# Optimization experiments

Hardware: AMD Instinct MI355X
Metric: run time of the kernel (lower is better)

Reference implementation:

```python
import jax, jax.numpy as jnp
import numpy as np
from jax import lax

B, N, C = 8, 2000, 81
MAX_INST = 100
MIN_CONF = 0.7
NMS_THR = 0.3
WINDOW = jnp.array([0.0, 0.0, 1.0, 1.0], jnp.float32)  # y1, x1, y2, x2
BBOX_STD = jnp.array([0.1, 0.1, 0.2, 0.2], jnp.float32)


def setup_inputs() -> dict:
    key = jax.random.key(0)
    k1, k2, k3 = jax.random.split(key, 3)
    # build valid boxes: sample coordinate pairs and sort so y1<=y2, x1<=x2
    yx = jax.random.uniform(k1, (B, N, 2, 2), dtype=jnp.float32)
    mins, maxs = yx.min(axis=2), yx.max(axis=2)
    rois = jnp.stack([mins[..., 0], mins[..., 1], maxs[..., 0], maxs[..., 1]], axis=-1)
    probs = jax.random.uniform(k2, (B, N, C), dtype=jnp.float32)
    deltas = jax.random.normal(k3, (B, N, C, 4), dtype=jnp.float32) * 0.5
    return {"rois": rois, "probs": probs, "deltas": deltas}


def _apply_box_deltas(boxes, deltas):
    # boxes: [N,4] (y1,x1,y2,x2); deltas: [N,4] (dy,dx,log_dh,log_dw)
    h = boxes[:, 2] - boxes[:, 0]
    w = boxes[:, 3] - boxes[:, 1]
    cy = boxes[:, 0] + 0.5 * h + deltas[:, 0] * h
    cx = boxes[:, 1] + 0.5 * w + deltas[:, 1] * w
    h = h * jnp.exp(deltas[:, 2])
    w = w * jnp.exp(deltas[:, 3])
    return jnp.stack([cy - 0.5 * h, cx - 0.5 * w, cy + 0.5 * h, cx + 0.5 * w], axis=1)


def _clip_boxes(boxes, window):
    wy1, wx1, wy2, wx2 = window
    y1 = jnp.clip(boxes[:, 0], wy1, wy2)
    x1 = jnp.clip(boxes[:, 1], wx1, wx2)
    y2 = jnp.clip(boxes[:, 2], wy1, wy2)
    x2 = jnp.clip(boxes[:, 3], wx1, wx2)
    return jnp.stack([y1, x1, y2, x2], axis=1)


def _pairwise_iou(boxes):
    # boxes: [N,4] -> [N,N]
    y1, x1, y2, x2 = boxes[:, 0], boxes[:, 1], boxes[:, 2], boxes[:, 3]
    area = (y2 - y1) * (x2 - x1)
    iy1 = jnp.maximum(y1[:, None], y1[None, :])
    ix1 = jnp.maximum(x1[:, None], x1[None, :])
    iy2 = jnp.minimum(y2[:, None], y2[None, :])
    ix2 = jnp.minimum(x2[:, None], x2[None, :])
    inter = jnp.maximum(iy2 - iy1, 0.0) * jnp.maximum(ix2 - ix1, 0.0)
    union = area[:, None] + area[None, :] - inter
    return inter / jnp.maximum(union, 1e-12)


def _refine_one(rois, probs, deltas):
    # rois [N,4], probs [N,C], deltas [N,C,4]
    class_ids = jnp.argmax(probs, axis=1)                      # [N]
    rng = jnp.arange(N)
    class_scores = probs[rng, class_ids]                       # [N]
    deltas_specific = deltas[rng, class_ids]                   # [N,4]
    refined = _apply_box_deltas(rois, deltas_specific * BBOX_STD)
    refined = _clip_boxes(refined, WINDOW)

    valid = (class_ids > 0) & (class_scores >= MIN_CONF)

    # sort by score descending (invalid entries pushed to the end)
    order = jnp.argsort(-jnp.where(valid, class_scores, -jnp.inf))
    boxes_s = refined[order]
    scores_s = class_scores[order]
    cls_s = class_ids[order]
    valid_s = valid[order]

    # per-class greedy NMS: suppress only within the same class
    iou = _pairwise_iou(boxes_s)                               # [N,N]
    suppress_mat = (iou > NMS_THR) & (cls_s[:, None] == cls_s[None, :])
    lower = jnp.arange(N)

    def body(i, keep):
        sup = suppress_mat[i] & keep[i] & (lower > i)
        return keep & ~sup

    keep = lax.fori_loop(0, N, body, valid_s)

    # per-class cap at MAX_INST (mirrors max_output_size in tf NMS)
    onehot = jax.nn.one_hot(cls_s, C, dtype=jnp.int32) * keep.astype(jnp.int32)[:, None]
    rank = jnp.cumsum(onehot, axis=0)[lower, cls_s]            # inclusive per-class rank
    keep = keep & (rank <= MAX_INST)

    # global top-k by score among kept, zero-padded
    final_scores = jnp.where(keep, scores_s, -jnp.inf)
    _, top_idx = lax.top_k(final_scores, MAX_INST)
    valid_top = keep[top_idx]
    box_out = jnp.where(valid_top[:, None], boxes_s[top_idx], 0.0)
    cls_out = jnp.where(valid_top, cls_s[top_idx].astype(jnp.float32), 0.0)
    sc_out = jnp.where(valid_top, scores_s[top_idx], 0.0)
    return jnp.concatenate([box_out, cls_out[:, None], sc_out[:, None]], axis=1)  # [MAX_INST,6]


def reference(rois, probs, deltas):
    return jax.vmap(_refine_one)(rois, probs, deltas)  # [B, MAX_INST, 6]
```

## Files before the change

### kernel.cpp

```cpp
#include <hip/hip_runtime.h>
#include <math.h>

#define BB 8
#define NN 2000
#define CC 81
#define NCLS 80
#define MAXI 100
#define MCLS 128
#define WCAP 128
#define KCAP 2048

static constexpr float kMinConf = 0.7f;
static constexpr float kNmsThr  = 0.3f;


__device__ __forceinline__ unsigned long long mkey(float s, int i) {
    return ((unsigned long long)__float_as_uint(s) << 32) | (unsigned int)(~(unsigned int)i);
}

__device__ __forceinline__ bool iou_gt_thr(float4 a, float aarea, float4 t) {
    float iy1 = fmaxf(a.x, t.x), ix1 = fmaxf(a.y, t.y);
    float iy2 = fminf(a.z, t.z), ix2 = fminf(a.w, t.w);
    float inter = fmaxf(iy2 - iy1, 0.f) * fmaxf(ix2 - ix1, 0.f);
    float tarea = (t.z - t.x) * (t.w - t.y);
    float uni = fmaxf(aarea + tarea - inter, 1e-12f);
    return inter > kNmsThr * uni;
}

__global__ void kA_refine(const float* __restrict__ rois,
                          const float* __restrict__ probs,
                          const float* __restrict__ deltas,
                          float* __restrict__ boxes,
                          float* __restrict__ sc,
                          int* __restrict__ cls,
                          float* __restrict__ outz) {
    int gtid = blockIdx.x * blockDim.x + threadIdx.x;
    if (gtid < BB * MAXI * 6) outz[gtid] = 0.f;

    int wid = gtid >> 6;
    int l = gtid & 63;

    const float* p = probs + (size_t)wid * CC;
    float v1 = p[l];
    int   i1 = l;
    int   c2 = l + 64;
    float v2 = (c2 < CC) ? p[c2] : -1.0f;
    float bv; int bi;
    if (v2 > v1) { bv = v2; bi = c2; } else { bv = v1; bi = i1; }

    #pragma unroll
    for (int off = 32; off; off >>= 1) {
        float ov = __shfl_xor(bv, off);
        int   oi = __shfl_xor(bi, off);
        if (ov > bv || (ov == bv && oi < bi)) { bv = ov; bi = oi; }
    }

    if (l == 0) {
        const float4 dl = *(const float4*)(deltas + ((size_t)wid * CC + bi) * 4);
        float dy = dl.x * 0.1f, dx = dl.y * 0.1f, dh = dl.z * 0.2f, dw = dl.w * 0.2f;
        const float4 r = *(const float4*)(rois + (size_t)wid * 4);
        float y1 = r.x, x1 = r.y, y2 = r.z, x2 = r.w;
        float h = y2 - y1, w = x2 - x1;
        float cy = y1 + 0.5f * h + dy * h;
        float cx = x1 + 0.5f * w + dx * w;
        float h2 = h * expf(dh);
        float w2 = w * expf(dw);
        float oy1 = fminf(fmaxf(cy - 0.5f * h2, 0.f), 1.f);
        float ox1 = fminf(fmaxf(cx - 0.5f * w2, 0.f), 1.f);
        float oy2 = fminf(fmaxf(cy + 0.5f * h2, 0.f), 1.f);
        float ox2 = fminf(fmaxf(cx + 0.5f * w2, 0.f), 1.f);
        bool valid = (bi > 0) && (bv >= kMinConf);
        float4 bx; bx.x = oy1; bx.y = ox1; bx.z = oy2; bx.w = ox2;
        ((float4*)boxes)[wid] = bx;
        sc[wid] = bv;
        cls[wid] = valid ? bi : 0;
    }
}

__global__ void __launch_bounds__(256) kB_nms(
        const float* __restrict__ boxes,
        const float* __restrict__ sc,
        const int* __restrict__ cls,
        int* __restrict__ kslot,
        unsigned long long* __restrict__ klist) {
    const int p = blockIdx.x;
    const int b = p / NCLS;
    const int cidx = p % NCLS;
    const int c = cidx + 1;
    const int tid = threadIdx.x;
    const int wv = tid >> 6;
    const int l = tid & 63;

    __shared__ unsigned long long wlist[4][WCAP];
    __shared__ int wcnt[4];
    __shared__ unsigned long long mk[MCLS];
    __shared__ float4 mbox[MCLS];

    const int* cl = cls + (size_t)b * NN;
    const float* ssc = sc + (size_t)b * NN;
    const float4* bxs = (const float4*)boxes + (size_t)b * NN;

    {
        int cnt = 0;
        const int base_row = wv * 500;
        for (int ch = 0; ch < 8; ++ch) {
            int idx = ch * 64 + l;
            bool inq = idx < 500;
            int r = base_row + idx;
            int ci = inq ? cl[r] : 0;
            bool pred = (ci == c);
            unsigned long long mask = __ballot(pred);
            if (pred) {
                int pos = cnt + __popcll(mask & ((1ull << l) - 1ull));
                if (pos < WCAP) wlist[wv][pos] = mkey(ssc[r], r);
            }
            cnt += __popcll(mask);
        }
        if (l == 0) wcnt[wv] = (cnt > WCAP) ? WCAP : cnt;
    }
    __syncthreads();

    int b0 = wcnt[0], b1 = wcnt[1], b2 = wcnt[2], b3 = wcnt[3];
    int myofs = (wv > 0 ? b0 : 0) + (wv > 1 ? b1 : 0) + (wv > 2 ? b2 : 0);
    int myn = wcnt[wv];
    int cnt_all = b0 + b1 + b2 + b3;
    if (cnt_all > MCLS) cnt_all = MCLS;
    if (l < myn && myofs + l < MCLS) mk[myofs + l] = wlist[wv][l];
    if (64 + l < myn && myofs + 64 + l < MCLS) mk[myofs + 64 + l] = wlist[wv][64 + l];
    __syncthreads();

    if (wv != 0) return;
    if (cnt_all == 0) {
        if (l == 0) kslot[b * NCLS + cidx] = 0;
        return;
    }
    const int cnt = cnt_all;

    {
        unsigned long long Ka = (l < cnt) ? mk[l] : 0ull;
        unsigned long long Kb = (64 + l < cnt) ? mk[64 + l] : 0ull;
        int ra = 0, rb = 0;
        for (int t = 0; t < cnt; ++t) {
            unsigned long long kt = mk[t];
            ra += (kt > Ka);
            rb += (kt > Kb);
        }
        if (l < cnt) mk[ra] = Ka;
        if (64 + l < cnt) mk[rb] = Kb;
    }

    for (int t = l; t < cnt; t += 64) {
        int i = (int)(~(unsigned int)mk[t]);
        mbox[t] = bxs[i];
    }

    unsigned long long kept0 = 0ull, kept1 = 0ull;
    {
        bool act = (l < cnt);
        float4 a = mbox[act ? l : 0];
        float aarea = (a.z - a.x) * (a.w - a.y);
        unsigned long long colmask = 0ull;
        int tend = min(64, cnt);
        for (int t = 0; t < tend; ++t) {
            float4 tb = mbox[t];
            if (t < l && act && iou_gt_thr(a, aarea, tb)) colmask |= (1ull << t);
        }
        unsigned long long kept = __ballot(act);
        while (true) {
            bool alive = act && ((colmask & kept) == 0ull);
            unsigned long long k2m = __ballot(alive);
            if (k2m == kept) break;
            kept = k2m;
        }
        kept0 = kept;
    }
    if (cnt > 64) {
        int m = 64 + l;
        bool act = (m < cnt);
        float4 a = mbox[act ? m : 0];
        float aarea = (a.z - a.x) * (a.w - a.y);
        bool presup = false;
        for (int t = 0; t < 64; ++t) {
            if ((kept0 >> t) & 1ull) {
                if (act && iou_gt_thr(a, aarea, mbox[t])) presup = true;
            }
        }
        unsigned long long colmask = 0ull;
        for (int t = 64; t < cnt; ++t) {
            float4 tb = mbox[t];
            if ((t - 64) < l && act && iou_gt_thr(a, aarea, tb)) colmask |= (1ull << (t - 64));
        }
        bool pre = act && !presup;
        unsigned long long kept = __ballot(pre);
        while (true) {
            bool alive = pre && ((colmask & kept) == 0ull);
            unsigned long long k2m = __ballot(alive);
            if (k2m == kept) break;
            kept = k2m;
        }
        kept1 = kept;
    }

    int nk0 = __popcll(kept0), nk1 = __popcll(kept1);
    unsigned long long* slot = klist + ((size_t)b * NCLS + cidx) * MCLS;
    if ((kept0 >> l) & 1ull)
        slot[__popcll(kept0 & ((1ull << l) - 1ull))] = mk[l];
    if (cnt > 64 && ((kept1 >> l) & 1ull))
        slot[nk0 + __popcll(kept1 & ((1ull << l) - 1ull))] = mk[64 + l];
    if (l == 0) kslot[b * NCLS + cidx] = nk0 + nk1;
}

__global__ void __launch_bounds__(512) kC_emit(
        const int* __restrict__ kslot,
        const unsigned long long* __restrict__ klist,
        const float* __restrict__ boxes,
        const int* __restrict__ cls,
        float* __restrict__ out) {
    const int b = blockIdx.x;
    const int tid = threadIdx.x;
    const int wv = tid >> 6;
    const int l = tid & 63;

    __shared__ unsigned long long keys[KCAP];
    __shared__ ulonglong2 cand2[256];
    __shared__ int hist[256];
    __shared__ int sbase[NCLS], scount[NCLS];
    __shared__ int Tsh, tbsh, candn;
    unsigned long long* cand = (unsigned long long*)cand2;

    if (tid < 256) hist[tid] = 0;
    if (tid == 0) candn = 0;

    if (wv == 0) {
        const int* ks = kslot + b * NCLS;
        int ns0 = ks[l];
        int ns1 = (l < NCLS - 64) ? ks[64 + l] : 0;
        int incA = ns0, incB = ns1;
        #pragma unroll
        for (int off = 1; off < 64; off <<= 1) {
            int oa = __shfl_up(incA, off);
            int ob = __shfl_up(incB, off);
            if (l >= off) { incA += oa; incB += ob; }
        }
        int total0 = __shfl(incA, 63);
        int T = total0 + __shfl(incB, 63);
        sbase[l] = incA - ns0;
        scount[l] = ns0;
        if (l < NCLS - 64) { sbase[64 + l] = total0 + incB - ns1; scount[64 + l] = ns1; }
        if (l == 0) Tsh = (T > KCAP) ? KCAP : T;
    }
    __syncthreads();
    const int T = Tsh;
    if (T == 0) return;

    const unsigned long long* kbase = klist + (size_t)b * NCLS * MCLS;
    for (int e = tid; e < NCLS * MCLS; e += 512) {
        unsigned long long v = kbase[e];
        int s = e >> 7, j = e & (MCLS - 1);
        if (j < scount[s]) keys[sbase[s] + j] = v;
    }
    __syncthreads();

    for (int t = tid; t < T; t += 512)
        atomicAdd(&hist[(int)((keys[t] >> 47) & 0xFF)], 1);
    __syncthreads();

    if (wv == 0) {
        int cum = 0, tb = 0, done = 0;
        for (int chunk = 3; chunk >= 0 && !done; --chunk) {
            int bkt = chunk * 64 + (63 - l);
            int s = hist[bkt];
            #pragma unroll
            for (int off = 1; off < 64; off <<= 1) {
                int o = __shfl_up(s, off);
                if (l >= off) s += o;
            }
            int chunktot = __shfl(s, 63);
            if (cum + chunktot >= MAXI) {
                unsigned long long m = __ballot(cum + s >= MAXI);
                int lane = __ffsll((long long)m) - 1;
                tb = chunk * 64 + (63 - lane);
                done = 1;
            } else {
                cum += chunktot;
            }
        }
        if (l == 0) tbsh = done ? tb : 0;
    }
    __syncthreads();
    const int tb = tbsh;

    for (int t = tid; t < ((T + 511) & ~511); t += 512) {
        bool pr = (t < T) && ((int)((keys[t] >> 47) & 0xFF) >= tb);
        unsigned long long m = __ballot(pr);
        int nb = __popcll(m);
        int basew = 0;
        if (l == 0 && nb) basew = atomicAdd(&candn, nb);
        basew = __shfl(basew, 0);
        if (pr) {
            int pos = basew + __popcll(m & ((1ull << l) - 1ull));
            if (pos < 512) cand[pos] = keys[t];
        }
    }
    __syncthreads();
    const int nc = candn;
    if (tid == 0 && nc < 512) cand[nc] = 0ull;
    __syncthreads();

    if (nc <= 512) {
        const int np = (nc + 1) >> 1;
        for (int s = tid; s < nc; s += 512) {
            unsigned long long myk = cand[s];
            int r = 0;
            for (int t = 0; t < np; ++t) {
                ulonglong2 kv = cand2[t];
                r += (int)(kv.x > myk);
                r += (int)(kv.y > myk);
            }
            if (r < MAXI) {
                int i = (int)(~(unsigned int)myk);
                float4 bx = ((const float4*)boxes)[(size_t)b * NN + i];
                float* o = out + ((size_t)b * MAXI + r) * 6;
                o[0] = bx.x; o[1] = bx.y; o[2] = bx.z; o[3] = bx.w;
                o[4] = (float)cls[(size_t)b * NN + i];
                o[5] = __uint_as_float((unsigned int)(myk >> 32));
            }
        }
    } else {
        for (int s = tid; s < T; s += 512) {
            unsigned long long myk = keys[s];
            int r = 0;
            for (int t = 0; t < T; ++t) r += (int)(keys[t] > myk);
            if (r < MAXI) {
                int i = (int)(~(unsigned int)myk);
                float4 bx = ((const float4*)boxes)[(size_t)b * NN + i];
                float* o = out + ((size_t)b * MAXI + r) * 6;
                o[0] = bx.x; o[1] = bx.y; o[2] = bx.z; o[3] = bx.w;
                o[4] = (float)cls[(size_t)b * NN + i];
                o[5] = __uint_as_float((unsigned int)(myk >> 32));
            }
        }
    }
}

extern "C" void kernel_launch(void* const* d_in, const int* in_sizes, int n_in,
                              void* d_out, int out_size, void* d_ws, size_t ws_size,
                              hipStream_t stream) {
    const float* rois   = (const float*)d_in[0];
    const float* probs  = (const float*)d_in[1];
    const float* deltas = (const float*)d_in[2];
    float* outp = (float*)d_out;

    char* ws = (char*)d_ws;
    float* boxes = (float*)(ws + 0);
    float* sc    = (float*)(ws + 256000);
    int*   cls   = (int*)  (ws + 320000);
    int*   kslot = (int*)  (ws + 384000);
    unsigned long long* klist = (unsigned long long*)(ws + 386624);

    {
        int blocks = (BB * NN * 64) / 256;
        kA_refine<<<blocks, 256, 0, stream>>>(rois, probs, deltas, boxes, sc, cls, outp);
    }
    {
        kB_nms<<<BB * NCLS, 256, 0, stream>>>(boxes, sc, cls, kslot, klist);
    }
    {
        kC_emit<<<BB, 512, 0, stream>>>(kslot, klist, boxes, cls, outp);
    }
}
```

Baseline: 35.37 us.

## Fuse NMS and emit kernels using release-store flags and spin-waiting emit blocks

Merges the per-class NMS kernel and the per-batch emit kernel into one launch. The emit blocks are appended after the NMS blocks and spin on per-class counters, which are initialised to -1 in the refine kernel and published with release atomics. This removes one kernel launch and its inter-kernel gap. In exchange, emit blocks drop from 512 to 256 threads, and correctness depends on the NMS blocks being scheduled before or alongside the spinning emit blocks, which risks deadlock or wasted spinning.

Measured after the change: 48.01 us. 1.36x slower.

```diff
diff --git a/kernel.cpp b/kernel.cpp
--- a/kernel.cpp
+++ b/kernel.cpp
@@ -33,9 +33,11 @@
                           float* __restrict__ boxes,
                           float* __restrict__ sc,
                           int* __restrict__ cls,
+                          int* __restrict__ kslot,
                           float* __restrict__ outz) {
     int gtid = blockIdx.x * blockDim.x + threadIdx.x;
     if (gtid < BB * MAXI * 6) outz[gtid] = 0.f;
+    if (gtid < BB * NCLS) kslot[gtid] = -1;
 
     int wid = gtid >> 6;
     int l = gtid & 63;
@@ -77,16 +79,14 @@
     }
 }
 
-__global__ void __launch_bounds__(256) kB_nms(
+__global__ void __launch_bounds__(256) k2_nms_emit(
         const float* __restrict__ boxes,
         const float* __restrict__ sc,
         const int* __restrict__ cls,
         int* __restrict__ kslot,
-        unsigned long long* __restrict__ klist) {
-    const int p = blockIdx.x;
-    const int b = p / NCLS;
-    const int cidx = p % NCLS;
-    const int c = cidx + 1;
+        unsigned long long* __restrict__ klist,
+        float* __restrict__ out) {
+    const int blk = blockIdx.x;
     const int tid = threadIdx.x;
     const int wv = tid >> 6;
     const int l = tid & 63;
@@ -95,146 +95,157 @@
     __shared__ int wcnt[4];
     __shared__ unsigned long long mk[MCLS];
     __shared__ float4 mbox[MCLS];
-
-    const int* cl = cls + (size_t)b * NN;
-    const float* ssc = sc + (size_t)b * NN;
-    const float4* bxs = (const float4*)boxes + (size_t)b * NN;
-
-    {
-        int cnt = 0;
-        const int base_row = wv * 500;
-        for (int ch = 0; ch < 8; ++ch) {
-            int idx = ch * 64 + l;
-            bool inq = idx < 500;
-            int r = base_row + idx;
-            int ci = inq ? cl[r] : 0;
-            bool pred = (ci == c);
-            unsigned long long mask = __ballot(pred);
-            if (pred) {
-                int pos = cnt + __popcll(mask & ((1ull << l) - 1ull));
-                if (pos < WCAP) wlist[wv][pos] = mkey(ssc[r], r);
-            }
-            cnt += __popcll(mask);
-        }
-        if (l == 0) wcnt[wv] = (cnt > WCAP) ? WCAP : cnt;
-    }
-    __syncthreads();
-
-    int b0 = wcnt[0], b1 = wcnt[1], b2 = wcnt[2], b3 = wcnt[3];
-    int myofs = (wv > 0 ? b0 : 0) + (wv > 1 ? b1 : 0) + (wv > 2 ? b2 : 0);
-    int myn = wcnt[wv];
-    int cnt_all = b0 + b1 + b2 + b3;
-    if (cnt_all > MCLS) cnt_all = MCLS;
-    if (l < myn && myofs + l < MCLS) mk[myofs + l] = wlist[wv][l];
-    if (64 + l < myn && myofs + 64 + l < MCLS) mk[myofs + 64 + l] = wlist[wv][64 + l];
-    __syncthreads();
-
-    if (wv != 0) return;
-    if (cnt_all == 0) {
-        if (l == 0) kslot[b * NCLS + cidx] = 0;
-        return;
-    }
-    const int cnt = cnt_all;
-
-    {
-        unsigned long long Ka = (l < cnt) ? mk[l] : 0ull;
-        unsigned long long Kb = (64 + l < cnt) ? mk[64 + l] : 0ull;
-        int ra = 0, rb = 0;
-        for (int t = 0; t < cnt; ++t) {
-            unsigned long long kt = mk[t];
-            ra += (kt > Ka);
-            rb += (kt > Kb);
-        }
-        if (l < cnt) mk[ra] = Ka;
-        if (64 + l < cnt) mk[rb] = Kb;
-    }
-
-    for (int t = l; t < cnt; t += 64) {
-        int i = (int)(~(unsigned int)mk[t]);
-        mbox[t] = bxs[i];
-    }
-
-    unsigned long long kept0 = 0ull, kept1 = 0ull;
-    {
-        bool act = (l < cnt);
-        float4 a = mbox[act ? l : 0];
-        float aarea = (a.z - a.x) * (a.w - a.y);
-        unsigned long long colmask = 0ull;
-        int tend = min(64, cnt);
-        for (int t = 0; t < tend; ++t) {
-            float4 tb = mbox[t];
-            if (t < l && act && iou_gt_thr(a, aarea, tb)) colmask |= (1ull << t);
-        }
-        unsigned long long kept = __ballot(act);
-        while (true) {
-            bool alive = act && ((colmask & kept) == 0ull);
-            unsigned long long k2m = __ballot(alive);
-            if (k2m == kept) break;
-            kept = k2m;
-        }
-        kept0 = kept;
-    }
-    if (cnt > 64) {
-        int m = 64 + l;
-        bool act = (m < cnt);
-        float4 a = mbox[act ? m : 0];
-        float aarea = (a.z - a.x) * (a.w - a.y);
-        bool presup = false;
-        for (int t = 0; t < 64; ++t) {
-            if ((kept0 >> t) & 1ull) {
-                if (act && iou_gt_thr(a, aarea, mbox[t])) presup = true;
-            }
-        }
-        unsigned long long colmask = 0ull;
-        for (int t = 64; t < cnt; ++t) {
-            float4 tb = mbox[t];
-            if ((t - 64) < l && act && iou_gt_thr(a, aarea, tb)) colmask |= (1ull << (t - 64));
-        }
-        bool pre = act && !presup;
-        unsigned long long kept = __ballot(pre);
-        while (true) {
-            bool alive = pre && ((colmask & kept) == 0ull);
-            unsigned long long k2m = __ballot(alive);
-            if (k2m == kept) break;
-            kept = k2m;
-        }
-        kept1 = kept;
-    }
-
-    int nk0 = __popcll(kept0), nk1 = __popcll(kept1);
-    unsigned long long* slot = klist + ((size_t)b * NCLS + cidx) * MCLS;
-    if ((kept0 >> l) & 1ull)
-        slot[__popcll(kept0 & ((1ull << l) - 1ull))] = mk[l];
-    if (cnt > 64 && ((kept1 >> l) & 1ull))
-        slot[nk0 + __popcll(kept1 & ((1ull << l) - 1ull))] = mk[64 + l];
-    if (l == 0) kslot[b * NCLS + cidx] = nk0 + nk1;
-}
-
-__global__ void __launch_bounds__(512) kC_emit(
-        const int* __restrict__ kslot,
-        const unsigned long long* __restrict__ klist,
-        const float* __restrict__ boxes,
-        const int* __restrict__ cls,
-        float* __restrict__ out) {
-    const int b = blockIdx.x;
-    const int tid = threadIdx.x;
-    const int wv = tid >> 6;
-    const int l = tid & 63;
-
     __shared__ unsigned long long keys[KCAP];
     __shared__ ulonglong2 cand2[256];
     __shared__ int hist[256];
-    __shared__ int sbase[NCLS], scount[NCLS];
+    __shared__ int sbase[NCLS], scnt[NCLS];
     __shared__ int Tsh, tbsh, candn;
     unsigned long long* cand = (unsigned long long*)cand2;
 
-    if (tid < 256) hist[tid] = 0;
+    if (blk < BB * NCLS) {
+        const int b = blk / NCLS;
+        const int cidx = blk % NCLS;
+        const int c = cidx + 1;
+
+        const int* cl = cls + (size_t)b * NN;
+        const float* ssc = sc + (size_t)b * NN;
+        const float4* bxs = (const float4*)boxes + (size_t)b * NN;
+
+        {
+            int cnt = 0;
+            const int base_row = wv * 500;
+            for (int ch = 0; ch < 8; ++ch) {
+                int idx = ch * 64 + l;
+                bool inq = idx < 500;
+                int r = base_row + idx;
+                int ci = inq ? cl[r] : 0;
+                bool pred = (ci == c);
+                unsigned long long mask = __ballot(pred);
+                if (pred) {
+                    int pos = cnt + __popcll(mask & ((1ull << l) - 1ull));
+                    if (pos < WCAP) wlist[wv][pos] = mkey(ssc[r], r);
+                }
+                cnt += __popcll(mask);
+            }
+            if (l == 0) wcnt[wv] = (cnt > WCAP) ? WCAP : cnt;
+        }
+        __syncthreads();
+
+        int b0 = wcnt[0], b1 = wcnt[1], b2 = wcnt[2], b3 = wcnt[3];
+        int myofs = (wv > 0 ? b0 : 0) + (wv > 1 ? b1 : 0) + (wv > 2 ? b2 : 0);
+        int myn = wcnt[wv];
+        int cnt_all = b0 + b1 + b2 + b3;
+        if (cnt_all > MCLS) cnt_all = MCLS;
+        if (l < myn && myofs + l < MCLS) mk[myofs + l] = wlist[wv][l];
+        if (64 + l < myn && myofs + 64 + l < MCLS) mk[myofs + 64 + l] = wlist[wv][64 + l];
+        __syncthreads();
+
+        if (wv != 0) return;
+        if (cnt_all == 0) {
+            if (l == 0)
+                __hip_atomic_store(&kslot[b * NCLS + cidx], 0,
+                                   __ATOMIC_RELEASE, __HIP_MEMORY_SCOPE_AGENT);
+            return;
+        }
+        const int cnt = cnt_all;
+
+        {
+            unsigned long long Ka = (l < cnt) ? mk[l] : 0ull;
+            unsigned long long Kb = (64 + l < cnt) ? mk[64 + l] : 0ull;
+            int ra = 0, rb = 0;
+            for (int t = 0; t < cnt; ++t) {
+                unsigned long long kt = mk[t];
+                ra += (kt > Ka);
+                rb += (kt > Kb);
+            }
+            if (l < cnt) mk[ra] = Ka;
+            if (64 + l < cnt) mk[rb] = Kb;
+        }
+        for (int t = l; t < cnt; t += 64) {
+            int i = (int)(~(unsigned int)mk[t]);
+            mbox[t] = bxs[i];
+        }
+
+        unsigned long long kept0 = 0ull, kept1 = 0ull;
+        {
+            bool act = (l < cnt);
+            float4 a = mbox[act ? l : 0];
+            float aarea = (a.z - a.x) * (a.w - a.y);
+            unsigned long long colmask = 0ull;
+            int tend = min(64, cnt);
+            for (int t = 0; t < tend; ++t) {
+                float4 tb = mbox[t];
+                if (t < l && act && iou_gt_thr(a, aarea, tb)) colmask |= (1ull << t);
+            }
+            unsigned long long kept = __ballot(act);
+            while (true) {
+                bool alive = act && ((colmask & kept) == 0ull);
+                unsigned long long k2m = __ballot(alive);
+                if (k2m == kept) break;
+                kept = k2m;
+            }
+            kept0 = kept;
+        }
+        if (cnt > 64) {
+            int m = 64 + l;
+            bool act = (m < cnt);
+            float4 a = mbox[act ? m : 0];
+            float aarea = (a.z - a.x) * (a.w - a.y);
+            bool presup = false;
+            for (int t = 0; t < 64; ++t) {
+                if ((kept0 >> t) & 1ull) {
+                    if (act && iou_gt_thr(a, aarea, mbox[t])) presup = true;
+                }
+            }
+            unsigned long long colmask = 0ull;
+            for (int t = 64; t < cnt; ++t) {
+                float4 tb = mbox[t];
+                if ((t - 64) < l && act && iou_gt_thr(a, aarea, tb)) colmask |= (1ull << (t - 64));
+            }
+            bool pre = act && !presup;
+            unsigned long long kept = __ballot(pre);
+            while (true) {
+                bool alive = pre && ((colmask & kept) == 0ull);
+                unsigned long long k2m = __ballot(alive);
+                if (k2m == kept) break;
+                kept = k2m;
+            }
+            kept1 = kept;
+        }
+
+        int nk0 = __popcll(kept0), nk1 = __popcll(kept1);
+        unsigned long long* slot = klist + ((size_t)b * NCLS + cidx) * MCLS;
+        if ((kept0 >> l) & 1ull)
+            slot[__popcll(kept0 & ((1ull << l) - 1ull))] = mk[l];
+        if (cnt > 64 && ((kept1 >> l) & 1ull))
+            slot[nk0 + __popcll(kept1 & ((1ull << l) - 1ull))] = mk[64 + l];
+        if (l == 0)
+            __hip_atomic_store(&kslot[b * NCLS + cidx], nk0 + nk1,
+                               __ATOMIC_RELEASE, __HIP_MEMORY_SCOPE_AGENT);
+        return;
+    }
+
+    const int b = blk - BB * NCLS;
+
+    {
+        int myc = 0;
+        while (true) {
+            myc = (tid < NCLS)
+                ? __hip_atomic_load(&kslot[b * NCLS + tid],
+                                    __ATOMIC_RELAXED, __HIP_MEMORY_SCOPE_AGENT)
+                : 0;
+            if (__syncthreads_and(myc >= 0)) break;
+        }
+        if (tid < NCLS) scnt[tid] = myc;
+    }
+    __threadfence();
+    if (tid < 256 && tid >= 0) hist[tid] = 0;
     if (tid == 0) candn = 0;
+    __syncthreads();
 
     if (wv == 0) {
-        const int* ks = kslot + b * NCLS;
-        int ns0 = ks[l];
-        int ns1 = (l < NCLS - 64) ? ks[64 + l] : 0;
+        int ns0 = scnt[l];
+        int ns1 = (l < NCLS - 64) ? scnt[64 + l] : 0;
         int incA = ns0, incB = ns1;
         #pragma unroll
         for (int off = 1; off < 64; off <<= 1) {
@@ -245,8 +256,7 @@
         int total0 = __shfl(incA, 63);
         int T = total0 + __shfl(incB, 63);
         sbase[l] = incA - ns0;
-        scount[l] = ns0;
-        if (l < NCLS - 64) { sbase[64 + l] = total0 + incB - ns1; scount[64 + l] = ns1; }
+        if (l < NCLS - 64) sbase[64 + l] = total0 + incB - ns1;
         if (l == 0) Tsh = (T > KCAP) ? KCAP : T;
     }
     __syncthreads();
@@ -254,14 +264,14 @@
     if (T == 0) return;
 
     const unsigned long long* kbase = klist + (size_t)b * NCLS * MCLS;
-    for (int e = tid; e < NCLS * MCLS; e += 512) {
+    for (int e = tid; e < NCLS * MCLS; e += 256) {
         unsigned long long v = kbase[e];
         int s = e >> 7, j = e & (MCLS - 1);
-        if (j < scount[s]) keys[sbase[s] + j] = v;
-    }
-    __syncthreads();
-
-    for (int t = tid; t < T; t += 512)
+        if (j < scnt[s]) keys[sbase[s] + j] = v;
+    }
+    __syncthreads();
+
+    for (int t = tid; t < T; t += 256)
         atomicAdd(&hist[(int)((keys[t] >> 47) & 0xFF)], 1);
     __syncthreads();
 
@@ -290,7 +300,7 @@
     __syncthreads();
     const int tb = tbsh;
 
-    for (int t = tid; t < ((T + 511) & ~511); t += 512) {
+    for (int t = tid; t < ((T + 255) & ~255); t += 256) {
         bool pr = (t < T) && ((int)((keys[t] >> 47) & 0xFF) >= tb);
         unsigned long long m = __ballot(pr);
         int nb = __popcll(m);
@@ -309,7 +319,7 @@
 
     if (nc <= 512) {
         const int np = (nc + 1) >> 1;
-        for (int s = tid; s < nc; s += 512) {
+        for (int s = tid; s < nc; s += 256) {
             unsigned long long myk = cand[s];
             int r = 0;
             for (int t = 0; t < np; ++t) {
@@ -327,7 +337,7 @@
             }
         }
     } else {
-        for (int s = tid; s < T; s += 512) {
+        for (int s = tid; s < T; s += 256) {
             unsigned long long myk = keys[s];
             int r = 0;
             for (int t = 0; t < T; ++t) r += (int)(keys[t] > myk);
@@ -360,12 +370,9 @@
 
     {
         int blocks = (BB * NN * 64) / 256;
-        kA_refine<<<blocks, 256, 0, stream>>>(rois, probs, deltas, boxes, sc, cls, outp);
+        kA_refine<<<blocks, 256, 0, stream>>>(rois, probs, deltas, boxes, sc, cls, kslot, outp);
     }
     {
-        kB_nms<<<BB * NCLS, 256, 0, stream>>>(boxes, sc, cls, kslot, klist);
-    }
-    {
-        kC_emit<<<BB, 512, 0, stream>>>(kslot, klist, boxes, cls, outp);
-    }
-}
+        k2_nms_emit<<<BB * NCLS + BB, 256, 0, stream>>>(boxes, sc, cls, kslot, klist, outp);
+    }
+}
```

## Replace per-class kept lists with per-box keep flags consumed by emit kernel

Applied to the files above, without the earlier changes.

The NMS kernel now writes a keep flag per box into a dense array instead of compacting kept keys into per-class slot lists with counts. The emit kernel, now launched with 1024 threads, scans all 2000 flags per batch, builds score keys and the histogram in a single pass, and no longer needs the prefix sum over class counts or the strided read of the sparse klist buffer. This removes the scattered klist traffic and one synchronised phase, at the cost of reading a dense flag array and a fallback ranking loop that now always scans the full 2048-entry key array.

After: 29.09 us. -17.7%, faster.

```diff
diff --git a/kernel.cpp b/kernel.cpp
--- a/kernel.cpp
+++ b/kernel.cpp
@@ -8,7 +8,6 @@
 #define MAXI 100
 #define MCLS 128
 #define WCAP 128
-#define KCAP 2048
 
 static constexpr float kMinConf = 0.7f;
 static constexpr float kNmsThr  = 0.3f;
@@ -33,9 +32,11 @@
                           float* __restrict__ boxes,
                           float* __restrict__ sc,
                           int* __restrict__ cls,
+                          int* __restrict__ kflag,
                           float* __restrict__ outz) {
     int gtid = blockIdx.x * blockDim.x + threadIdx.x;
     if (gtid < BB * MAXI * 6) outz[gtid] = 0.f;
+    if (gtid < BB * NN) kflag[gtid] = 0;
 
     int wid = gtid >> 6;
     int l = gtid & 63;
@@ -81,8 +82,7 @@
         const float* __restrict__ boxes,
         const float* __restrict__ sc,
         const int* __restrict__ cls,
-        int* __restrict__ kslot,
-        unsigned long long* __restrict__ klist) {
+        int* __restrict__ kflag) {
     const int p = blockIdx.x;
     const int b = p / NCLS;
     const int cidx = p % NCLS;
@@ -130,10 +130,7 @@
     __syncthreads();
 
     if (wv != 0) return;
-    if (cnt_all == 0) {
-        if (l == 0) kslot[b * NCLS + cidx] = 0;
-        return;
-    }
+    if (cnt_all == 0) return;
     const int cnt = cnt_all;
 
     {
@@ -154,7 +151,7 @@
         mbox[t] = bxs[i];
     }
 
-    unsigned long long kept0 = 0ull, kept1 = 0ull;
+    unsigned long long kept0 = 0ull;
     {
         bool act = (l < cnt);
         float4 a = mbox[act ? l : 0];
@@ -173,6 +170,8 @@
             kept = k2m;
         }
         kept0 = kept;
+        bool alive = act && ((colmask & kept0) == 0ull);
+        if (alive) kflag[(size_t)b * NN + (int)(~(unsigned int)mk[l])] = 1;
     }
     if (cnt > 64) {
         int m = 64 + l;
@@ -198,21 +197,14 @@
             if (k2m == kept) break;
             kept = k2m;
         }
-        kept1 = kept;
-    }
-
-    int nk0 = __popcll(kept0), nk1 = __popcll(kept1);
-    unsigned long long* slot = klist + ((size_t)b * NCLS + cidx) * MCLS;
-    if ((kept0 >> l) & 1ull)
-        slot[__popcll(kept0 & ((1ull << l) - 1ull))] = mk[l];
-    if (cnt > 64 && ((kept1 >> l) & 1ull))
-        slot[nk0 + __popcll(kept1 & ((1ull << l) - 1ull))] = mk[64 + l];
-    if (l == 0) kslot[b * NCLS + cidx] = nk0 + nk1;
-}
-
-__global__ void __launch_bounds__(512) kC_emit(
-        const int* __restrict__ kslot,
-        const unsigned long long* __restrict__ klist,
+        bool alive = pre && ((colmask & kept) == 0ull);
+        if (alive) kflag[(size_t)b * NN + (int)(~(unsigned int)mk[64 + l])] = 1;
+    }
+}
+
+__global__ void __launch_bounds__(1024) kC_emit(
+        const int* __restrict__ kflag,
+        const float* __restrict__ sc,
         const float* __restrict__ boxes,
         const int* __restrict__ cls,
         float* __restrict__ out) {
@@ -221,49 +213,28 @@
     const int wv = tid >> 6;
     const int l = tid & 63;
 
-    __shared__ unsigned long long keys[KCAP];
+    __shared__ unsigned long long keys[2048];
     __shared__ ulonglong2 cand2[256];
     __shared__ int hist[256];
-    __shared__ int sbase[NCLS], scount[NCLS];
-    __shared__ int Tsh, tbsh, candn;
+    __shared__ int Tcnt, tbsh, candn;
     unsigned long long* cand = (unsigned long long*)cand2;
 
     if (tid < 256) hist[tid] = 0;
-    if (tid == 0) candn = 0;
-
-    if (wv == 0) {
-        const int* ks = kslot + b * NCLS;
-        int ns0 = ks[l];
-        int ns1 = (l < NCLS - 64) ? ks[64 + l] : 0;
-        int incA = ns0, incB = ns1;
-        #pragma unroll
-        for (int off = 1; off < 64; off <<= 1) {
-            int oa = __shfl_up(incA, off);
-            int ob = __shfl_up(incB, off);
-            if (l >= off) { incA += oa; incB += ob; }
-        }
-        int total0 = __shfl(incA, 63);
-        int T = total0 + __shfl(incB, 63);
-        sbase[l] = incA - ns0;
-        scount[l] = ns0;
-        if (l < NCLS - 64) { sbase[64 + l] = total0 + incB - ns1; scount[64 + l] = ns1; }
-        if (l == 0) Tsh = (T > KCAP) ? KCAP : T;
-    }
-    __syncthreads();
-    const int T = Tsh;
+    if (tid < 48) keys[2000 + tid] = 0ull;
+    if (tid == 0) { Tcnt = 0; candn = 0; }
+    __syncthreads();
+
+    for (int i = tid; i < NN; i += 1024) {
+        int f = kflag[(size_t)b * NN + i];
+        unsigned long long k = f ? mkey(sc[(size_t)b * NN + i], i) : 0ull;
+        keys[i] = k;
+        if (f) atomicAdd(&hist[(int)((k >> 47) & 0xFF)], 1);
+        unsigned long long m = __ballot(f != 0);
+        if (l == 0 && m) atomicAdd(&Tcnt, __popcll(m));
+    }
+    __syncthreads();
+    const int T = Tcnt;
     if (T == 0) return;
-
-    const unsigned long long* kbase = klist + (size_t)b * NCLS * MCLS;
-    for (int e = tid; e < NCLS * MCLS; e += 512) {
-        unsigned long long v = kbase[e];
-        int s = e >> 7, j = e & (MCLS - 1);
-        if (j < scount[s]) keys[sbase[s] + j] = v;
-    }
-    __syncthreads();
-
-    for (int t = tid; t < T; t += 512)
-        atomicAdd(&hist[(int)((keys[t] >> 47) & 0xFF)], 1);
-    __syncthreads();
 
     if (wv == 0) {
         int cum = 0, tb = 0, done = 0;
@@ -290,16 +261,16 @@
     __syncthreads();
     const int tb = tbsh;
 
-    for (int t = tid; t < ((T + 511) & ~511); t += 512) {
-        bool pr = (t < T) && ((int)((keys[t] >> 47) & 0xFF) >= tb);
+    for (int i = tid; i < NN; i += 1024) {
+        unsigned long long k = keys[i];
+        bool pr = (k != 0ull) && ((int)((k >> 47) & 0xFF) >= tb);
         unsigned long long m = __ballot(pr);
-        int nb = __popcll(m);
         int basew = 0;
-        if (l == 0 && nb) basew = atomicAdd(&candn, nb);
+        if (l == 0 && m) basew = atomicAdd(&candn, __popcll(m));
         basew = __shfl(basew, 0);
         if (pr) {
             int pos = basew + __popcll(m & ((1ull << l) - 1ull));
-            if (pos < 512) cand[pos] = keys[t];
+            if (pos < 512) cand[pos] = k;
         }
     }
     __syncthreads();
@@ -309,7 +280,7 @@
 
     if (nc <= 512) {
         const int np = (nc + 1) >> 1;
-        for (int s = tid; s < nc; s += 512) {
+        for (int s = tid; s < nc; s += 1024) {
             unsigned long long myk = cand[s];
             int r = 0;
             for (int t = 0; t < np; ++t) {
@@ -327,10 +298,15 @@
             }
         }
     } else {
-        for (int s = tid; s < T; s += 512) {
+        for (int s = tid; s < NN; s += 1024) {
             unsigned long long myk = keys[s];
+            if (myk == 0ull) continue;
             int r = 0;
-            for (int t = 0; t < T; ++t) r += (int)(keys[t] > myk);
+            for (int t = 0; t < 1024; ++t) {
+                ulonglong2 kv = ((ulonglong2*)keys)[t];
+                r += (int)(kv.x > myk);
+                r += (int)(kv.y > myk);
+            }
             if (r < MAXI) {
                 int i = (int)(~(unsigned int)myk);
                 float4 bx = ((const float4*)boxes)[(size_t)b * NN + i];
@@ -355,17 +331,16 @@
     float* boxes = (float*)(ws + 0);
     float* sc    = (float*)(ws + 256000);
     int*   cls   = (int*)  (ws + 320000);
-    int*   kslot = (int*)  (ws + 384000);
-    unsigned long long* klist = (unsigned long long*)(ws + 386624);
+    int*   kflag = (int*)  (ws + 384000);
 
     {
         int blocks = (BB * NN * 64) / 256;
-        kA_refine<<<blocks, 256, 0, stream>>>(rois, probs, deltas, boxes, sc, cls, outp);
-    }
-    {
-        kB_nms<<<BB * NCLS, 256, 0, stream>>>(boxes, sc, cls, kslot, klist);
-    }
-    {
-        kC_emit<<<BB, 512, 0, stream>>>(kslot, klist, boxes, cls, outp);
-    }
-}
+        kA_refine<<<blocks, 256, 0, stream>>>(rois, probs, deltas, boxes, sc, cls, kflag, outp);
+    }
+    {
+        kB_nms<<<BB * NCLS, 256, 0, stream>>>(boxes, sc, cls, kflag);
+    }
+    {
+        kC_emit<<<BB, 1024, 0, stream>>>(kflag, sc, boxes, cls, outp);
+    }
+}
```
